# Kernel optimization log

Hardware: AMD Instinct MI355X
Metric: run time of the kernel (lower is better)

The kernel has to match this reference:

```python
import jax, jax.numpy as jnp
import numpy as np

B, C, D, H, W = 4, 256, 16, 64, 64


def setup_inputs() -> dict:
    key = jax.random.key(0)
    ks = jax.random.split(key, 9)
    s = 1.0 / np.sqrt(C)
    return {
        "x": jax.random.normal(ks[0], (B, C, H, W), dtype=jnp.float32),
        "Wq": jax.random.normal(ks[1], (D, C), dtype=jnp.float32) * s,
        "bq": jax.random.normal(ks[2], (D,), dtype=jnp.float32) * 0.01,
        "Wk": jax.random.normal(ks[3], (D, C), dtype=jnp.float32) * s,
        "bk": jax.random.normal(ks[4], (D,), dtype=jnp.float32) * 0.01,
        "Wv": jax.random.normal(ks[5], (D, C), dtype=jnp.float32) * s,
        "bv": jax.random.normal(ks[6], (D,), dtype=jnp.float32) * 0.01,
        "Wo": jax.random.normal(ks[7], (C, D), dtype=jnp.float32) / np.sqrt(D),
        "bo": jax.random.normal(ks[8], (C,), dtype=jnp.float32) * 0.01,
    }


def reference(x, Wq, bq, Wk, bk, Wv, bv, Wo, bo):
    b, c, h, w = x.shape
    n = h * w
    xf = x.reshape(b, c, n)                                   # [B,C,N]
    # 1x1 convs == channel-mixing matmuls
    q = jnp.einsum("bcn,dc->bdn", xf, Wq) + bq[:, None]        # [B,D,N]
    k = jnp.einsum("bcn,dc->bdn", xf, Wk) + bk[:, None]
    v = jnp.einsum("bcn,dc->bdn", xf, Wv) + bv[:, None]
    # attention_map[b, i, j] = softmax_j(q_i . k_j)  (NO 1/sqrt(d) scale)
    scores = jnp.einsum("bdi,bdj->bij", q, k)                  # [B,N,N]
    attn = jax.nn.softmax(scores, axis=-1)
    # attended[b, d, i] = sum_j v[b,d,j] * attn[b,i,j]
    av = jnp.einsum("bdj,bij->bdi", v, attn)                   # [B,D,N]
    out = jnp.einsum("bdn,cd->bcn", av, Wo) + bo[:, None]      # [B,C,N]
    return out.reshape(b, c, h, w)
```

## Files before the change

kernel.cpp:

```cpp
#include <hip/hip_runtime.h>
#include <hip/hip_bf16.h>

typedef unsigned short u16;
typedef unsigned int u32;
typedef float f32x4 __attribute__((ext_vector_type(4)));
typedef short bf16x8 __attribute__((ext_vector_type(8)));

#define LOG2E 1.4426950408889634f

static __device__ __forceinline__ u16 f2bf(float f){
  __hip_bfloat16 h = __float2bfloat16(f);
  return __builtin_bit_cast(u16, h);
}
static __device__ __forceinline__ float bf2f(u16 u){
  __hip_bfloat16 h = __builtin_bit_cast(__hip_bfloat16, u);
  return __bfloat162float(h);
}
static __device__ __forceinline__ float fexp2(float x){
#if __has_builtin(__builtin_amdgcn_exp2f)
  return __builtin_amdgcn_exp2f(x);
#else
  return exp2f(x);
#endif
}
static __device__ __forceinline__ u32 pack2(float a, float b){
  return (u32)f2bf(a) | ((u32)f2bf(b) << 16);
}
static __device__ __forceinline__ f32x4 mf(bf16x8 a, bf16x8 b, f32x4 c){
  return __builtin_amdgcn_mfma_f32_16x16x32_bf16(a, b, c, 0, 0, 0);
}

__global__ __launch_bounds__(256, 2) void qkv_kernel(
    const float* __restrict__ x,
    const float* __restrict__ Wq, const float* __restrict__ bq,
    const float* __restrict__ Wk, const float* __restrict__ bk,
    const float* __restrict__ Wv, const float* __restrict__ bv,
    u16* __restrict__ qh, u16* __restrict__ ql,
    u16* __restrict__ kcat, u16* __restrict__ vT)
{
  __shared__ float wlds[16*256];
  int t = threadIdx.x;
  int nt = blockIdx.x, b = blockIdx.y, m = blockIdx.z;
  const float* W    = (m==0) ? Wq : (m==1) ? Wk : Wv;
  const float* bias = (m==0) ? bq : (m==1) ? bk : bv;
  for (int idx = t; idx < 16*256; idx += 256) {
    int d = idx >> 8, c = idx & 255;
    int cg = c >> 6, cc4 = (c >> 2) & 15, j = c & 3;
    int pos = (d << 8) + (cg << 6) + ((cc4 ^ cg) << 2) + j;
    wlds[pos] = W[d*256 + c];
  }
  __syncthreads();
  int w = t >> 6, lane = t & 63;
  int nl = lane & 15, cg = lane >> 4;
  int n = nt*64 + w*16 + nl;
  float acc[16];
  #pragma unroll
  for (int d = 0; d < 16; ++d) acc[d] = 0.f;
  const float* xb = x + (b << 20) + n;
  const float4* wl4 = (const float4*)wlds;
  #pragma unroll 4
  for (int cc4 = 0; cc4 < 16; ++cc4) {
    int c0 = cg*64 + cc4*4;
    float x0 = xb[(c0+0) << 12];
    float x1 = xb[(c0+1) << 12];
    float x2 = xb[(c0+2) << 12];
    float x3 = xb[(c0+3) << 12];
    int f4b = (cg << 4) + (cc4 ^ cg);
    #pragma unroll
    for (int d = 0; d < 16; ++d) {
      float4 wv = wl4[(d << 6) + f4b];
      acc[d] += wv.x*x0 + wv.y*x1 + wv.z*x2 + wv.w*x3;
    }
  }
  #pragma unroll
  for (int d = 0; d < 16; ++d) {
    acc[d] += __shfl_xor(acc[d], 16, 64);
    acc[d] += __shfl_xor(acc[d], 32, 64);
  }
  if (m == 2) {
    #pragma unroll
    for (int jj = 0; jj < 4; ++jj) {
      int d = cg*4 + jj;
      vT[((size_t)((b*16 + d)) << 12) + n] = f2bf(acc[d] + bias[d]);
    }
  } else {
    int d0 = (cg & 1) * 8, lo = cg >> 1;
    alignas(16) u16 vals[8];
    #pragma unroll
    for (int jj = 0; jj < 8; ++jj) {
      int d = d0 + jj;
      float v_ = acc[d] + bias[d];
      u16 h = f2bf(v_);
      vals[jj] = lo ? f2bf(v_ - bf2f(h)) : h;
    }
    u16* dst;
    if (m == 0) {
      u16* base = lo ? ql : qh;
      dst = base + (((size_t)(b << 12) + n) << 4) + d0;
    } else {
      dst = kcat + (((size_t)(b << 12) + n) << 5) + cg*8;
    }
    *(int4*)dst = *(const int4*)vals;
  }
}

struct Frags { bf16x8 ac0,ac1,ac2,ac3, v0,v1; };

static __device__ __forceinline__ Frags loadFrags(
  const u16* __restrict__ kc, const u16* __restrict__ vp,
  int kb, int i, int g)
{
  Frags f;
  const u16* a0 = kc + (kb + i)*32 + g*8;
  f.ac0 = *(const bf16x8*)(a0);
  f.ac1 = *(const bf16x8*)(a0 + 512);
  f.ac2 = *(const bf16x8*)(a0 + 1024);
  f.ac3 = *(const bf16x8*)(a0 + 1536);
  const u16* v0p = vp + kb + g*8;
  f.v0 = *(const bf16x8*)(v0p);
  f.v1 = *(const bf16x8*)(v0p + 32);
  return f;
}

__global__ __launch_bounds__(256, 2) void attn_kernel(
    const u16* __restrict__ qh, const u16* __restrict__ ql,
    const u16* __restrict__ kcat, const u16* __restrict__ vT,
    float* __restrict__ av_part, float* __restrict__ l_part)
{
  __shared__ char plds[4*2048];
  int tid = threadIdx.x, wid = tid >> 6, lane = tid & 63;
  int g = lane >> 4, i = lane & 15;
  int b = blockIdx.y, s = blockIdx.z;
  int nsplit = gridDim.z;
  int iters = 64 / nsplit;
  int qidx = blockIdx.x*64 + wid*16 + i;
  char* myp = plds + wid*2048;
  int rowb = i*128;
  int mi = (i & 7) << 4;

  bf16x8 Bqh = *(const bf16x8*)(qh + ((size_t)((b << 12) + qidx))*16 + ((g & 1) << 3));
  bf16x8 Bql = *(const bf16x8*)(ql + ((size_t)((b << 12) + qidx))*16 + ((g & 1) << 3));
  if (g >= 2) {
    #pragma unroll
    for (int e = 0; e < 8; ++e) Bql[e] = 0;
  }
  const u16* kc = kcat + (size_t)b*4096*32;
  const u16* vp = vT   + ((size_t)(b*16 + i) << 12);

  f32x4 av = {0.f,0.f,0.f,0.f};
  float lsum = 0.f;
  int kb0 = s*(iters*64);
  Frags cu = loadFrags(kc, vp, kb0, i, g);
  #pragma unroll 2
  for (int it = 0; it < iters; ++it) {
    int kb = kb0 + it*64;
    int kbn = (it+1 < iters) ? (kb + 64) : kb;
    Frags nx = loadFrags(kc, vp, kbn, i, g);
    f32x4 z4 = {0.f,0.f,0.f,0.f};
    f32x4 s0 = mf(cu.ac0, Bqh, z4); s0 = mf(cu.ac0, Bql, s0);
    f32x4 s1 = mf(cu.ac1, Bqh, z4); s1 = mf(cu.ac1, Bql, s1);
    f32x4 s2 = mf(cu.ac2, Bqh, z4); s2 = mf(cu.ac2, Bql, s2);
    f32x4 s3 = mf(cu.ac3, Bqh, z4); s3 = mf(cu.ac3, Bql, s3);
    f32x4 p0, p1, p2, p3;
    #pragma unroll
    for (int r = 0; r < 4; ++r) {
      p0[r] = fexp2(s0[r]*LOG2E);
      p1[r] = fexp2(s1[r]*LOG2E);
      p2[r] = fexp2(s2[r]*LOG2E);
      p3[r] = fexp2(s3[r]*LOG2E);
    }
    lsum += (p0[0]+p0[1]+p0[2]+p0[3]) + (p1[0]+p1[1]+p1[2]+p1[3])
          + (p2[0]+p2[1]+p2[2]+p2[3]) + (p3[0]+p3[1]+p3[2]+p3[3]);
    *(uint2*)(myp + rowb + (((8*g)      ) ^ mi)) =
        (uint2){ pack2(p0[0], p0[1]), pack2(p0[2], p0[3]) };
    *(uint2*)(myp + rowb + (((8*g) + 32 ) ^ mi)) =
        (uint2){ pack2(p1[0], p1[1]), pack2(p1[2], p1[3]) };
    *(uint2*)(myp + rowb + (((8*g) + 64 ) ^ mi)) =
        (uint2){ pack2(p2[0], p2[1]), pack2(p2[2], p2[3]) };
    *(uint2*)(myp + rowb + (((8*g) + 96 ) ^ mi)) =
        (uint2){ pack2(p3[0], p3[1]), pack2(p3[2], p3[3]) };
    bf16x8 Bp0 = *(const bf16x8*)(myp + rowb + (( 0 + 16*g) ^ mi));
    bf16x8 Bp1 = *(const bf16x8*)(myp + rowb + ((64 + 16*g) ^ mi));
    av = mf(cu.v0, Bp0, av);
    av = mf(cu.v1, Bp1, av);
    cu = nx;
  }
  float lt = lsum;
  lt += __shfl_xor(lt, 16, 64);
  lt += __shfl_xor(lt, 32, 64);
  float* avp = av_part + ((size_t)((s*4 + b)*16) << 12);
  #pragma unroll
  for (int r = 0; r < 4; ++r)
    avp[((size_t)(4*g + r) << 12) + qidx] = av[r];
  if (lane < 16)
    l_part[((size_t)((s*4 + b)) << 12) + qidx] = lt;
}

__global__ __launch_bounds__(256, 4) void outproj_kernel(
    const float* __restrict__ av_part, const float* __restrict__ l_part,
    const float* __restrict__ Wo, const float* __restrict__ bo,
    float* __restrict__ out, int nsplit)
{
  __shared__ float wl[16][16];
  __shared__ float bol[16];
  int t = threadIdx.x;
  int ct = blockIdx.x, ntile = blockIdx.y, b = blockIdx.z;
  wl[t >> 4][t & 15] = Wo[(ct*16 + (t >> 4))*16 + (t & 15)];
  if (t < 16) bol[t] = bo[ct*16 + t];
  __syncthreads();
  int n = ntile*256 + t;
  float lsum = 0.f;
  for (int s = 0; s < nsplit; ++s)
    lsum += l_part[((size_t)(s*4 + b) << 12) + n];
  float inv = 1.f / lsum;
  float avv[16];
  #pragma unroll
  for (int d = 0; d < 16; ++d) avv[d] = 0.f;
  for (int s = 0; s < nsplit; ++s) {
    #pragma unroll
    for (int d = 0; d < 16; ++d)
      avv[d] += av_part[((size_t)((s*4 + b)*16 + d) << 12) + n];
  }
  #pragma unroll
  for (int d = 0; d < 16; ++d) avv[d] *= inv;
  #pragma unroll
  for (int cc = 0; cc < 16; ++cc) {
    float o = bol[cc];
    #pragma unroll
    for (int d = 0; d < 16; ++d) o += wl[cc][d] * avv[d];
    out[((size_t)(b*256 + ct*16 + cc) << 12) + n] = o;
  }
}

extern "C" void kernel_launch(void* const* d_in, const int* in_sizes, int n_in,
                              void* d_out, int out_size, void* d_ws, size_t ws_size,
                              hipStream_t stream) {
  (void)in_sizes; (void)n_in; (void)out_size;
  const float* x  = (const float*)d_in[0];
  const float* Wq = (const float*)d_in[1];
  const float* bq = (const float*)d_in[2];
  const float* Wk = (const float*)d_in[3];
  const float* bk = (const float*)d_in[4];
  const float* Wv = (const float*)d_in[5];
  const float* bv = (const float*)d_in[6];
  const float* Wo = (const float*)d_in[7];
  const float* bo = (const float*)d_in[8];
  float* out = (float*)d_out;
  char* ws = (char*)d_ws;

  const size_t fixed = 2621440;
  const size_t per_split = 1048576 + 65536;
  int nsplit = 8;
  while (nsplit > 1 && fixed + (size_t)nsplit*per_split > ws_size) nsplit >>= 1;

  u16* qh   = (u16*)(ws + 0);
  u16* ql   = (u16*)(ws + 524288);
  u16* kcat = (u16*)(ws + 1048576);
  u16* vT   = (u16*)(ws + 2097152);
  float* av_part = (float*)(ws + fixed);
  float* l_part  = (float*)(ws + fixed + (size_t)nsplit*1048576);

  qkv_kernel<<<dim3(64, 4, 3), dim3(256), 0, stream>>>(
      x, Wq, bq, Wk, bk, Wv, bv, qh, ql, kcat, vT);
  attn_kernel<<<dim3(64, 4, nsplit), dim3(256), 0, stream>>>(
      qh, ql, kcat, vT, av_part, l_part);
  outproj_kernel<<<dim3(16, 16, 4), dim3(256), 0, stream>>>(
      av_part, l_part, Wo, bo, out, nsplit);
}
```

Before: 151.8 us.

## Double-buffer attention P tiles, prefetch x loads, and store av_part query-major

The attention loop now alternates between two per-wave LDS tiles and two fragment sets, so loads for chunk it+2 can overlap compute on chunk it+1 and LDS write-after-read hazards between consecutive chunks go away. The qkv kernel software-prefetches the next four x channels, and both it and the attention kernel raise launch bounds to 4 blocks per CU. av_part moves from a d-major to a query-major layout, so attention writes one float4 per lane and outproj reads four float4s instead of 16 strided scalars. The risks are higher register and LDS pressure under the tighter occupancy bound, which could cause spills, and the iteration count must be even.

```diff
diff --git a/kernel.cpp b/kernel.cpp
--- a/kernel.cpp
+++ b/kernel.cpp
@@ -30,7 +30,7 @@
   return __builtin_amdgcn_mfma_f32_16x16x32_bf16(a, b, c, 0, 0, 0);
 }
 
-__global__ __launch_bounds__(256, 2) void qkv_kernel(
+__global__ __launch_bounds__(256, 4) void qkv_kernel(
     const float* __restrict__ x,
     const float* __restrict__ Wq, const float* __restrict__ bq,
     const float* __restrict__ Wk, const float* __restrict__ bk,
@@ -58,19 +58,24 @@
   for (int d = 0; d < 16; ++d) acc[d] = 0.f;
   const float* xb = x + (b << 20) + n;
   const float4* wl4 = (const float4*)wlds;
-  #pragma unroll 4
+  int c0 = cg*64;
+  float x0 = xb[(c0+0) << 12], x1 = xb[(c0+1) << 12];
+  float x2 = xb[(c0+2) << 12], x3 = xb[(c0+3) << 12];
+  #pragma unroll
   for (int cc4 = 0; cc4 < 16; ++cc4) {
-    int c0 = cg*64 + cc4*4;
-    float x0 = xb[(c0+0) << 12];
-    float x1 = xb[(c0+1) << 12];
-    float x2 = xb[(c0+2) << 12];
-    float x3 = xb[(c0+3) << 12];
+    float n0=0.f, n1=0.f, n2=0.f, n3=0.f;
+    if (cc4 < 15) {
+      int cn = cg*64 + (cc4+1)*4;
+      n0 = xb[(cn+0) << 12]; n1 = xb[(cn+1) << 12];
+      n2 = xb[(cn+2) << 12]; n3 = xb[(cn+3) << 12];
+    }
     int f4b = (cg << 4) + (cc4 ^ cg);
     #pragma unroll
     for (int d = 0; d < 16; ++d) {
       float4 wv = wl4[(d << 6) + f4b];
       acc[d] += wv.x*x0 + wv.y*x1 + wv.z*x2 + wv.w*x3;
     }
+    x0 = n0; x1 = n1; x2 = n2; x3 = n3;
   }
   #pragma unroll
   for (int d = 0; d < 16; ++d) {
@@ -122,19 +127,53 @@
   return f;
 }
 
-__global__ __launch_bounds__(256, 2) void attn_kernel(
+static __device__ __forceinline__ void computeChunk(
+  const Frags& cu, char* tile, bf16x8 Bqh, bf16x8 Bql,
+  f32x4& av, float& lsum, int rowb, int mi, int g)
+{
+  f32x4 z4 = {0.f,0.f,0.f,0.f};
+  f32x4 s0 = mf(cu.ac0, Bqh, z4); s0 = mf(cu.ac0, Bql, s0);
+  f32x4 s1 = mf(cu.ac1, Bqh, z4); s1 = mf(cu.ac1, Bql, s1);
+  f32x4 s2 = mf(cu.ac2, Bqh, z4); s2 = mf(cu.ac2, Bql, s2);
+  f32x4 s3 = mf(cu.ac3, Bqh, z4); s3 = mf(cu.ac3, Bql, s3);
+  f32x4 p0, p1, p2, p3;
+  #pragma unroll
+  for (int r = 0; r < 4; ++r) {
+    p0[r] = fexp2(s0[r]*LOG2E);
+    p1[r] = fexp2(s1[r]*LOG2E);
+    p2[r] = fexp2(s2[r]*LOG2E);
+    p3[r] = fexp2(s3[r]*LOG2E);
+  }
+  lsum += (p0[0]+p0[1]+p0[2]+p0[3]) + (p1[0]+p1[1]+p1[2]+p1[3])
+        + (p2[0]+p2[1]+p2[2]+p2[3]) + (p3[0]+p3[1]+p3[2]+p3[3]);
+  *(uint2*)(tile + rowb + (((8*g)      ) ^ mi)) =
+      (uint2){ pack2(p0[0], p0[1]), pack2(p0[2], p0[3]) };
+  *(uint2*)(tile + rowb + (((8*g) + 32 ) ^ mi)) =
+      (uint2){ pack2(p1[0], p1[1]), pack2(p1[2], p1[3]) };
+  *(uint2*)(tile + rowb + (((8*g) + 64 ) ^ mi)) =
+      (uint2){ pack2(p2[0], p2[1]), pack2(p2[2], p2[3]) };
+  *(uint2*)(tile + rowb + (((8*g) + 96 ) ^ mi)) =
+      (uint2){ pack2(p3[0], p3[1]), pack2(p3[2], p3[3]) };
+  bf16x8 Bp0 = *(const bf16x8*)(tile + rowb + (( 0 + 16*g) ^ mi));
+  bf16x8 Bp1 = *(const bf16x8*)(tile + rowb + ((64 + 16*g) ^ mi));
+  av = mf(cu.v0, Bp0, av);
+  av = mf(cu.v1, Bp1, av);
+}
+
+__global__ __launch_bounds__(256, 4) void attn_kernel(
     const u16* __restrict__ qh, const u16* __restrict__ ql,
     const u16* __restrict__ kcat, const u16* __restrict__ vT,
     float* __restrict__ av_part, float* __restrict__ l_part)
 {
-  __shared__ char plds[4*2048];
+  __shared__ char plds[4*4096];
   int tid = threadIdx.x, wid = tid >> 6, lane = tid & 63;
   int g = lane >> 4, i = lane & 15;
   int b = blockIdx.y, s = blockIdx.z;
   int nsplit = gridDim.z;
   int iters = 64 / nsplit;
   int qidx = blockIdx.x*64 + wid*16 + i;
-  char* myp = plds + wid*2048;
+  char* myp0 = plds + wid*4096;
+  char* myp1 = myp0 + 2048;
   int rowb = i*128;
   int mi = (i & 7) << 4;
 
@@ -150,50 +189,22 @@
   f32x4 av = {0.f,0.f,0.f,0.f};
   float lsum = 0.f;
   int kb0 = s*(iters*64);
-  Frags cu = loadFrags(kc, vp, kb0, i, g);
-  #pragma unroll 2
-  for (int it = 0; it < iters; ++it) {
-    int kb = kb0 + it*64;
-    int kbn = (it+1 < iters) ? (kb + 64) : kb;
-    Frags nx = loadFrags(kc, vp, kbn, i, g);
-    f32x4 z4 = {0.f,0.f,0.f,0.f};
-    f32x4 s0 = mf(cu.ac0, Bqh, z4); s0 = mf(cu.ac0, Bql, s0);
-    f32x4 s1 = mf(cu.ac1, Bqh, z4); s1 = mf(cu.ac1, Bql, s1);
-    f32x4 s2 = mf(cu.ac2, Bqh, z4); s2 = mf(cu.ac2, Bql, s2);
-    f32x4 s3 = mf(cu.ac3, Bqh, z4); s3 = mf(cu.ac3, Bql, s3);
-    f32x4 p0, p1, p2, p3;
-    #pragma unroll
-    for (int r = 0; r < 4; ++r) {
-      p0[r] = fexp2(s0[r]*LOG2E);
-      p1[r] = fexp2(s1[r]*LOG2E);
-      p2[r] = fexp2(s2[r]*LOG2E);
-      p3[r] = fexp2(s3[r]*LOG2E);
-    }
-    lsum += (p0[0]+p0[1]+p0[2]+p0[3]) + (p1[0]+p1[1]+p1[2]+p1[3])
-          + (p2[0]+p2[1]+p2[2]+p2[3]) + (p3[0]+p3[1]+p3[2]+p3[3]);
-    *(uint2*)(myp + rowb + (((8*g)      ) ^ mi)) =
-        (uint2){ pack2(p0[0], p0[1]), pack2(p0[2], p0[3]) };
-    *(uint2*)(myp + rowb + (((8*g) + 32 ) ^ mi)) =
-        (uint2){ pack2(p1[0], p1[1]), pack2(p1[2], p1[3]) };
-    *(uint2*)(myp + rowb + (((8*g) + 64 ) ^ mi)) =
-        (uint2){ pack2(p2[0], p2[1]), pack2(p2[2], p2[3]) };
-    *(uint2*)(myp + rowb + (((8*g) + 96 ) ^ mi)) =
-        (uint2){ pack2(p3[0], p3[1]), pack2(p3[2], p3[3]) };
-    bf16x8 Bp0 = *(const bf16x8*)(myp + rowb + (( 0 + 16*g) ^ mi));
-    bf16x8 Bp1 = *(const bf16x8*)(myp + rowb + ((64 + 16*g) ^ mi));
-    av = mf(cu.v0, Bp0, av);
-    av = mf(cu.v1, Bp1, av);
-    cu = nx;
+  Frags fA = loadFrags(kc, vp, kb0,      i, g);
+  Frags fB = loadFrags(kc, vp, kb0 + 64, i, g);
+  for (int it = 0; it < iters; it += 2) {
+    computeChunk(fA, myp0, Bqh, Bql, av, lsum, rowb, mi, g);
+    if (it + 2 < iters) fA = loadFrags(kc, vp, kb0 + (it+2)*64, i, g);
+    computeChunk(fB, myp1, Bqh, Bql, av, lsum, rowb, mi, g);
+    if (it + 3 < iters) fB = loadFrags(kc, vp, kb0 + (it+3)*64, i, g);
   }
   float lt = lsum;
   lt += __shfl_xor(lt, 16, 64);
   lt += __shfl_xor(lt, 32, 64);
-  float* avp = av_part + ((size_t)((s*4 + b)*16) << 12);
-  #pragma unroll
-  for (int r = 0; r < 4; ++r)
-    avp[((size_t)(4*g + r) << 12) + qidx] = av[r];
+  float* avp = av_part + ((size_t)(s*4 + b) << 16);
+  float4 st = { av[0], av[1], av[2], av[3] };
+  *(float4*)(avp + ((size_t)qidx << 4) + (g << 2)) = st;
   if (lane < 16)
-    l_part[((size_t)((s*4 + b)) << 12) + qidx] = lt;
+    l_part[((size_t)(s*4 + b) << 12) + qidx] = lt;
 }
 
 __global__ __launch_bounds__(256, 4) void outproj_kernel(
@@ -217,9 +228,14 @@
   #pragma unroll
   for (int d = 0; d < 16; ++d) avv[d] = 0.f;
   for (int s = 0; s < nsplit; ++s) {
-    #pragma unroll
-    for (int d = 0; d < 16; ++d)
-      avv[d] += av_part[((size_t)((s*4 + b)*16 + d) << 12) + n];
+    const float4* ap = (const float4*)(av_part + ((size_t)(s*4 + b) << 16)
+                                      + ((size_t)n << 4));
+    #pragma unroll
+    for (int q_ = 0; q_ < 4; ++q_) {
+      float4 a = ap[q_];
+      avv[q_*4+0] += a.x; avv[q_*4+1] += a.y;
+      avv[q_*4+2] += a.z; avv[q_*4+3] += a.w;
+    }
   }
   #pragma unroll
   for (int d = 0; d < 16; ++d) avv[d] *= inv;
```

Measured after the change: 201.2 us. 1.33x slower.
